# Kernel tuning notes

Measured on AMD Instinct MI355X. Metric: run time of the kernel, lower is better.

## Reference

```python
import jax, jax.numpy as jnp
import numpy as np

B, CI, CO, F, H, W = 8, 32, 64, 4, 64, 64


def _grid(h, w):
    # channel 0 varies along W so dx = coords[0,1,0]-coords[0,0,0] is the uniform spacing
    xs = jnp.linspace(0.0, 1.0, w, dtype=jnp.float32)
    ys = jnp.linspace(0.0, 1.0, h, dtype=jnp.float32)
    gy, gx = jnp.meshgrid(ys, xs, indexing='ij')
    return jnp.stack([gx, gy], axis=-1)  # [h, w, 2]


def _trapz(x, dx, axis):
    # trapezoidal rule with uniform spacing dx along `axis`
    return dx * (x.sum(axis=axis) - 0.5 * (jnp.take(x, 0, axis=axis) + jnp.take(x, -1, axis=axis)))


def integral_2d(x, dx, dim1, dim2):
    # 2D quadrature over dims dim1 < dim2 (reduce dim2 first so dim1 index stays valid)
    return _trapz(_trapz(x, dx, dim2), dx, dim1)


def setup_inputs() -> dict:
    key = jax.random.key(0)
    k1, k2, k3 = jax.random.split(key, 3)
    fan_in_scale = 1.0 / np.sqrt(CI * 2)  # kaiming-ish init scale
    return {
        'v': jax.random.normal(k1, (B, CI, H, W), dtype=jnp.float32),
        'v_coords': _grid(H, W),
        'target_coords': _grid(H, W),
        'Wx': jax.random.normal(k2, (F, CO, CI, 2), dtype=jnp.float32) * fan_in_scale,
        'Wy': jax.random.normal(k3, (F, CO, CI, 2), dtype=jnp.float32) * fan_in_scale,
    }


def reference(v, v_coords, target_coords, Wx, Wy):
    # v: [b, i, h, w]; coords: [h, w, 2]; Wx/Wy: [f, o, i, 2]
    vp = jnp.transpose(v, (0, 2, 3, 1))                 # [b, h, w, i]
    dx = v_coords[0, 1, 0] - v_coords[0, 0, 0]
    iv = integral_2d(vp, dx, 1, 2)                      # [b, i]
    # == einsum('foid,hwd->hwfoi', Wx, target_coords) then 'hwfoi,bi->bhwfo'
    scaled = jnp.einsum('foid,bi,hwd->bhwfo', Wx, iv, target_coords, optimize=True)
    # == einsum('foid,hwd->hwfoi', Wy, v_coords) then 'hwfoi,bhwi->bhwfo'
    Wyvp = jnp.einsum('foid,hwd,bhwi->bhwfo', Wy, v_coords, vp, optimize=True)
    iw = integral_2d(Wyvp, dx, 1, 2)                    # [b, f, o]
    up = scaled + iw[:, None, None]                     # [b, h, w, f, o]
    up = up.sum(axis=3)                                 # [b, h, w, o]
    return jnp.transpose(up, (0, 3, 1, 2))              # [b, o, h, w]
```

## Files before the change

kernel.cpp:

```cpp
#include <hip/hip_runtime.h>
#include <hip/hip_bf16.h>

#define B_  8
#define CI_ 32
#define CO_ 64
#define F_  4
#define H_  64
#define W_  64

__global__ __launch_bounds__(256) void k_reduce(
    const float* __restrict__ v, const float* __restrict__ vc,
    float* __restrict__ iv, float* __restrict__ T) {
  const int bi = blockIdx.x;
  const int tid = threadIdx.x;
  const float* vp = v + (size_t)bi * (H_ * W_);

  float s0 = 0.f, s1 = 0.f, s2 = 0.f;
  for (int p = tid; p < H_ * W_; p += 256) {
    int h = p >> 6;
    int w = p & 63;
    float wgt = ((h == 0 || h == H_ - 1) ? 0.5f : 1.0f) *
                ((w == 0 || w == W_ - 1) ? 0.5f : 1.0f);
    float val = vp[p] * wgt;
    float cx = vc[2 * p];
    float cy = vc[2 * p + 1];
    s0 += val;
    s1 += val * cx;
    s2 += val * cy;
  }

  for (int off = 32; off > 0; off >>= 1) {
    s0 += __shfl_down(s0, off, 64);
    s1 += __shfl_down(s1, off, 64);
    s2 += __shfl_down(s2, off, 64);
  }
  __shared__ float red[4][3];
  int wave = tid >> 6;
  int lane = tid & 63;
  if (lane == 0) {
    red[wave][0] = s0; red[wave][1] = s1; red[wave][2] = s2;
  }
  __syncthreads();
  if (tid == 0) {
    float t0 = red[0][0] + red[1][0] + red[2][0] + red[3][0];
    float t1 = red[0][1] + red[1][1] + red[2][1] + red[3][1];
    float t2 = red[0][2] + red[1][2] + red[2][2] + red[3][2];
    float dx = vc[2] - vc[0];
    float sc = dx * dx;
    iv[bi]        = t0 * sc;
    T[2 * bi]     = t1 * sc;
    T[2 * bi + 1] = t2 * sc;
  }
}

__global__ __launch_bounds__(256) void k_out_fused(
    const float* __restrict__ tc, const float* __restrict__ Wx,
    const float* __restrict__ Wy, const float* __restrict__ iv,
    const float* __restrict__ T, float* __restrict__ out) {
  const int blk = blockIdx.x;
  const int tid = threadIdx.x;
  const int bo  = blk >> 2;
  const int b   = bo >> 6;
  const int o   = bo & 63;

  float sx0 = 0.f, sx1 = 0.f, c = 0.f;
  if (tid < CI_ * F_) {
    int i = tid & (CI_ - 1);
    int f = tid >> 5;
    float ivbi = iv[b * CI_ + i];
    float t0 = T[(b * CI_ + i) * 2];
    float t1 = T[(b * CI_ + i) * 2 + 1];
    int base = ((f * CO_ + o) * CI_ + i) * 2;
    float2 wx = *(const float2*)(Wx + base);
    float2 wy = *(const float2*)(Wy + base);
    sx0 = wx.x * ivbi;
    sx1 = wx.y * ivbi;
    c   = wy.x * t0 + wy.y * t1;
  }
  for (int off = 32; off > 0; off >>= 1) {
    sx0 += __shfl_down(sx0, off, 64);
    sx1 += __shfl_down(sx1, off, 64);
    c   += __shfl_down(c,   off, 64);
  }
  __shared__ float red[2][3];
  __shared__ float bc[3];
  int wave = tid >> 6;
  int lane = tid & 63;
  if (wave < 2 && lane == 0) {
    red[wave][0] = sx0; red[wave][1] = sx1; red[wave][2] = c;
  }
  __syncthreads();
  if (tid == 0) {
    bc[0] = red[0][0] + red[1][0];
    bc[1] = red[0][1] + red[1][1];
    bc[2] = red[0][2] + red[1][2];
  }
  __syncthreads();
  const float SX0 = bc[0], SX1 = bc[1], C = bc[2];

  int p4 = (blk & 3) * 256 + tid;
  int h  = p4 >> 4;
  int w4 = p4 & 15;

  const float4* tcp = (const float4*)(tc + (size_t)(h * W_ + w4 * 4) * 2);
  float4 t0v = tcp[0];
  float4 t1v = tcp[1];

  float4 r;
  r.x = t0v.x * SX0 + t0v.y * SX1 + C;
  r.y = t0v.z * SX0 + t0v.w * SX1 + C;
  r.z = t1v.x * SX0 + t1v.y * SX1 + C;
  r.w = t1v.z * SX0 + t1v.w * SX1 + C;

  ((float4*)out)[(size_t)bo * 1024 + p4] = r;
}

extern "C" void kernel_launch(void* const* d_in, const int* in_sizes, int n_in,
                              void* d_out, int out_size, void* d_ws, size_t ws_size,
                              hipStream_t stream) {
  const float* v  = (const float*)d_in[0];
  const float* vc = (const float*)d_in[1];
  const float* tc = (const float*)d_in[2];
  const float* Wx = (const float*)d_in[3];
  const float* Wy = (const float*)d_in[4];
  float* out = (float*)d_out;

  float* iv = (float*)d_ws;
  float* T  = iv + B_ * CI_;

  k_reduce<<<B_ * CI_, 256, 0, stream>>>(v, vc, iv, T);
  k_out_fused<<<B_ * CO_ * 4, 256, 0, stream>>>(tc, Wx, Wy, iv, T, out);
}
```

Baseline: 71.15 us.

## Fuse reduce and output kernels into one cooperative launch with grid sync

Merges the two kernels into a single cooperative kernel of B*CO blocks. The first B*CI blocks do the per-channel reductions, a grid-wide sync follows, and then every block computes its own (b,o) coefficients and writes the full 64x64 plane in four unrolled iterations. This removes the second kernel launch and the dependency gap between the launches. In exchange it pays for a grid barrier and the overhead of a cooperative launch, runs with four times fewer output blocks, and leaves half the blocks idle during the reduction phase.

After: 135.6 us. +90.6%, slower.

```diff
diff --git a/kernel.cpp b/kernel.cpp
--- a/kernel.cpp
+++ b/kernel.cpp
@@ -1,5 +1,8 @@
 #include <hip/hip_runtime.h>
 #include <hip/hip_bf16.h>
+#include <hip/hip_cooperative_groups.h>
+
+namespace cg = cooperative_groups;
 
 #define B_  8
 #define CI_ 32
@@ -8,60 +11,60 @@
 #define H_  64
 #define W_  64
 
-__global__ __launch_bounds__(256) void k_reduce(
+__global__ __launch_bounds__(256) void k_fused(
     const float* __restrict__ v, const float* __restrict__ vc,
-    float* __restrict__ iv, float* __restrict__ T) {
-  const int bi = blockIdx.x;
+    const float* __restrict__ tc, const float* __restrict__ Wx,
+    const float* __restrict__ Wy, float* __restrict__ iv,
+    float* __restrict__ T, float* __restrict__ out) {
+  cg::grid_group grid = cg::this_grid();
+  const int blk = blockIdx.x;
   const int tid = threadIdx.x;
-  const float* vp = v + (size_t)bi * (H_ * W_);
+  const int wave = tid >> 6;
+  const int lane = tid & 63;
 
-  float s0 = 0.f, s1 = 0.f, s2 = 0.f;
-  for (int p = tid; p < H_ * W_; p += 256) {
-    int h = p >> 6;
-    int w = p & 63;
-    float wgt = ((h == 0 || h == H_ - 1) ? 0.5f : 1.0f) *
-                ((w == 0 || w == W_ - 1) ? 0.5f : 1.0f);
-    float val = vp[p] * wgt;
-    float cx = vc[2 * p];
-    float cy = vc[2 * p + 1];
-    s0 += val;
-    s1 += val * cx;
-    s2 += val * cy;
+  __shared__ float red[4][3];
+  __shared__ float bc[3];
+
+  if (blk < B_ * CI_) {
+    const float* vp = v + (size_t)blk * (H_ * W_);
+    float s0 = 0.f, s1 = 0.f, s2 = 0.f;
+    for (int p = tid; p < H_ * W_; p += 256) {
+      int h = p >> 6;
+      int w = p & 63;
+      float wgt = ((h == 0 || h == H_ - 1) ? 0.5f : 1.0f) *
+                  ((w == 0 || w == W_ - 1) ? 0.5f : 1.0f);
+      float val = vp[p] * wgt;
+      s0 += val;
+      s1 += val * vc[2 * p];
+      s2 += val * vc[2 * p + 1];
+    }
+    for (int off = 32; off > 0; off >>= 1) {
+      s0 += __shfl_down(s0, off, 64);
+      s1 += __shfl_down(s1, off, 64);
+      s2 += __shfl_down(s2, off, 64);
+    }
+    if (lane == 0) {
+      red[wave][0] = s0; red[wave][1] = s1; red[wave][2] = s2;
+    }
+    __syncthreads();
+    if (tid == 0) {
+      float t0 = red[0][0] + red[1][0] + red[2][0] + red[3][0];
+      float t1 = red[0][1] + red[1][1] + red[2][1] + red[3][1];
+      float t2 = red[0][2] + red[1][2] + red[2][2] + red[3][2];
+      float dx = vc[2] - vc[0];
+      float sc = dx * dx;
+      iv[blk]        = t0 * sc;
+      T[2 * blk]     = t1 * sc;
+      T[2 * blk + 1] = t2 * sc;
+      __threadfence();
+    }
   }
 
-  for (int off = 32; off > 0; off >>= 1) {
-    s0 += __shfl_down(s0, off, 64);
-    s1 += __shfl_down(s1, off, 64);
-    s2 += __shfl_down(s2, off, 64);
-  }
-  __shared__ float red[4][3];
-  int wave = tid >> 6;
-  int lane = tid & 63;
-  if (lane == 0) {
-    red[wave][0] = s0; red[wave][1] = s1; red[wave][2] = s2;
-  }
-  __syncthreads();
-  if (tid == 0) {
-    float t0 = red[0][0] + red[1][0] + red[2][0] + red[3][0];
-    float t1 = red[0][1] + red[1][1] + red[2][1] + red[3][1];
-    float t2 = red[0][2] + red[1][2] + red[2][2] + red[3][2];
-    float dx = vc[2] - vc[0];
-    float sc = dx * dx;
-    iv[bi]        = t0 * sc;
-    T[2 * bi]     = t1 * sc;
-    T[2 * bi + 1] = t2 * sc;
-  }
-}
+  grid.sync();
 
-__global__ __launch_bounds__(256) void k_out_fused(
-    const float* __restrict__ tc, const float* __restrict__ Wx,
-    const float* __restrict__ Wy, const float* __restrict__ iv,
-    const float* __restrict__ T, float* __restrict__ out) {
-  const int blk = blockIdx.x;
-  const int tid = threadIdx.x;
-  const int bo  = blk >> 2;
-  const int b   = bo >> 6;
-  const int o   = bo & 63;
+  const int bo = blk;
+  const int b  = bo >> 6;
+  const int o  = bo & 63;
 
   float sx0 = 0.f, sx1 = 0.f, c = 0.f;
   if (tid < CI_ * F_) {
@@ -82,10 +85,7 @@
     sx1 += __shfl_down(sx1, off, 64);
     c   += __shfl_down(c,   off, 64);
   }
-  __shared__ float red[2][3];
-  __shared__ float bc[3];
-  int wave = tid >> 6;
-  int lane = tid & 63;
+  __syncthreads();
   if (wave < 2 && lane == 0) {
     red[wave][0] = sx0; red[wave][1] = sx1; red[wave][2] = c;
   }
@@ -98,21 +98,22 @@
   __syncthreads();
   const float SX0 = bc[0], SX1 = bc[1], C = bc[2];
 
-  int p4 = (blk & 3) * 256 + tid;
-  int h  = p4 >> 4;
-  int w4 = p4 & 15;
-
-  const float4* tcp = (const float4*)(tc + (size_t)(h * W_ + w4 * 4) * 2);
-  float4 t0v = tcp[0];
-  float4 t1v = tcp[1];
-
-  float4 r;
-  r.x = t0v.x * SX0 + t0v.y * SX1 + C;
-  r.y = t0v.z * SX0 + t0v.w * SX1 + C;
-  r.z = t1v.x * SX0 + t1v.y * SX1 + C;
-  r.w = t1v.z * SX0 + t1v.w * SX1 + C;
-
-  ((float4*)out)[(size_t)bo * 1024 + p4] = r;
+  float4* outp = (float4*)out + (size_t)bo * 1024;
+#pragma unroll
+  for (int r = 0; r < 4; ++r) {
+    int p4 = r * 256 + tid;
+    int h  = p4 >> 4;
+    int w4 = p4 & 15;
+    const float4* tcp = (const float4*)(tc + (size_t)(h * W_ + w4 * 4) * 2);
+    float4 t0v = tcp[0];
+    float4 t1v = tcp[1];
+    float4 rr;
+    rr.x = t0v.x * SX0 + t0v.y * SX1 + C;
+    rr.y = t0v.z * SX0 + t0v.w * SX1 + C;
+    rr.z = t1v.x * SX0 + t1v.y * SX1 + C;
+    rr.w = t1v.z * SX0 + t1v.w * SX1 + C;
+    outp[p4] = rr;
+  }
 }
 
 extern "C" void kernel_launch(void* const* d_in, const int* in_sizes, int n_in,
@@ -128,6 +129,8 @@
   float* iv = (float*)d_ws;
   float* T  = iv + B_ * CI_;
 
-  k_reduce<<<B_ * CI_, 256, 0, stream>>>(v, vc, iv, T);
-  k_out_fused<<<B_ * CO_ * 4, 256, 0, stream>>>(tc, Wx, Wy, iv, T, out);
+  void* args[] = {(void*)&v, (void*)&vc, (void*)&tc, (void*)&Wx,
+                  (void*)&Wy, (void*)&iv, (void*)&T, (void*)&out};
+  hipLaunchCooperativeKernel((const void*)k_fused, dim3(B_ * CO_), dim3(256),
+                             args, 0, stream);
 }
```
